# Performance work log

Measured on AMD Instinct MI355X. Metric: run time of the kernel, lower is better.

Reference implementation:

```python
import jax, jax.numpy as jnp
import numpy as np
import math

IN_FEATURES = 256
OUT_FEATURES = 128
B, N = 4, 4096


def setup_inputs() -> dict:
    key = jax.random.key(0)
    ks = jax.random.split(key, 8)
    h = jax.random.normal(ks[0], (B, N, IN_FEATURES), dtype=jnp.float32)
    adj = jax.random.randint(ks[1], (B, N, N), 0, 2, dtype=jnp.int32)
    # Linear params (torch nn.Linear: y = x @ W.T + b)
    s = 1.0 / math.sqrt(IN_FEATURES)
    Wq = jax.random.uniform(ks[2], (OUT_FEATURES, IN_FEATURES), jnp.float32, -s, s)
    bq = jax.random.uniform(ks[3], (OUT_FEATURES,), jnp.float32, -s, s)
    Wk = jax.random.uniform(ks[4], (OUT_FEATURES, IN_FEATURES), jnp.float32, -s, s)
    bk = jax.random.uniform(ks[5], (OUT_FEATURES,), jnp.float32, -s, s)
    Wv = jax.random.uniform(ks[6], (OUT_FEATURES, IN_FEATURES), jnp.float32, -s, s)
    bv = jax.random.uniform(ks[7], (OUT_FEATURES,), jnp.float32, -s, s)
    return {"h": h, "adj": adj, "Wq": Wq, "bq": bq, "Wk": Wk, "bk": bk, "Wv": Wv, "bv": bv}


def reference(h, adj, Wq, bq, Wk, bk, Wv, bv):
    # QKV projections: [B, N, D]
    q = jnp.einsum('bnf,df->bnd', h, Wq) + bq
    k = jnp.einsum('bnf,df->bnd', h, Wk) + bk
    v = jnp.einsum('bnf,df->bnd', h, Wv) + bv
    # Dense scores [B, N, N], scaled
    scores = jnp.einsum('bnd,bmd->bnm', q, k) / math.sqrt(OUT_FEATURES)
    neg = jnp.float32(-9e15)
    scores = jnp.where(adj > 0, scores, neg)
    probs = jax.nn.softmax(scores, axis=-1)
    return jnp.einsum('bnm,bmd->bnd', probs, v)
```

## Files before the change

### kernel.cpp

```cpp
#include <hip/hip_runtime.h>
#include <stdint.h>
#include <math.h>

#define NB 4
#define NN 4096
#define NF 256
#define ND 128
#define KVB 32
#define NR (NB * NN)
#define QKVE ((size_t)NR * ND)

typedef __bf16 bf16x8 __attribute__((ext_vector_type(8)));
typedef __bf16 bf16x4v __attribute__((ext_vector_type(4)));
typedef float f32x4 __attribute__((ext_vector_type(4)));
typedef unsigned short u16x4 __attribute__((ext_vector_type(4)));

__device__ __forceinline__ unsigned short f2bf(float f) {
    union { float f; uint32_t u; } v; v.f = f;
    uint32_t r = (v.u + 0x7FFFu + ((v.u >> 16) & 1u)) >> 16;
    return (unsigned short)r;
}
__device__ __forceinline__ bf16x8 lds_read16(const unsigned short* base, int byte_off) {
    return *reinterpret_cast<const bf16x8*>(reinterpret_cast<const char*>(base) + byte_off);
}
__device__ __forceinline__ void gld_lds16(const void* g, void* l) {
    __builtin_amdgcn_global_load_lds(
        (const __attribute__((address_space(1))) void*)g,
        (__attribute__((address_space(3))) void*)l, 16, 0, 0);
}

__global__ __launch_bounds__(256) void pack_proj(
    const int* __restrict__ adj, unsigned long long* __restrict__ pm64,
    const float* __restrict__ h,
    const float* __restrict__ Wq, const float* __restrict__ bq,
    const float* __restrict__ Wk, const float* __restrict__ bk,
    const float* __restrict__ Wv, const float* __restrict__ bv,
    unsigned short* __restrict__ qo, unsigned short* __restrict__ ko,
    unsigned short* __restrict__ vs, float qscale)
{
    __shared__ unsigned short h_lds[64 * 128];
    __shared__ unsigned short w_lds[128 * 128];

    const int tid = threadIdx.x;
    const int lane = tid & 63;

    if (blockIdx.x < 1024) {
        const int w = tid >> 6;
        const size_t base = ((size_t)blockIdx.x * 4 + w) * 256;
        for (int o = 0; o < 32; ++o) {
            const size_t wb = base + o * 8;
            int v[8];
#pragma unroll
            for (int u = 0; u < 8; ++u)
                v[u] = adj[(wb + u) * 64 + lane];
            unsigned long long m[8];
#pragma unroll
            for (int u = 0; u < 8; ++u)
                m[u] = __ballot(v[u] != 0);
            if (lane == 0) {
#pragma unroll
                for (int u = 0; u < 8; u += 2) {
                    ulonglong2 st; st.x = m[u]; st.y = m[u + 1];
                    *reinterpret_cast<ulonglong2*>(pm64 + wb + u) = st;
                }
            }
        }
        return;
    }

    const int idx = blockIdx.x - 1024;
    const int proj = idx >> 8;
    const int R0 = (idx & 255) * 64;
    const int wv = tid >> 6;
    const int l15 = lane & 15;
    const int lhi = lane >> 4;

    const float* W    = proj == 0 ? Wq : (proj == 1 ? Wk : Wv);
    const float* bias = proj == 0 ? bq : (proj == 1 ? bk : bv);
    const float scale = proj == 0 ? qscale : 1.0f;

    f32x4 acc[8];
#pragma unroll
    for (int i = 0; i < 8; ++i) acc[i] = f32x4{0.f, 0.f, 0.f, 0.f};

    for (int kc = 0; kc < 2; ++kc) {
        const int c0 = kc * 128;
        __syncthreads();
#pragma unroll
        for (int p = 0; p < 8; ++p) {
            int i2 = p * 256 + tid;
            int row = i2 >> 5;
            int seg = i2 & 31;
            f32x4 hv = *reinterpret_cast<const f32x4*>(h + (size_t)(R0 + row) * NF + c0 + seg * 4);
            u16x4 hb;
            hb[0] = f2bf(hv[0]); hb[1] = f2bf(hv[1]); hb[2] = f2bf(hv[2]); hb[3] = f2bf(hv[3]);
            int byte = (row * 256 + seg * 8) ^ ((row & 7) << 4);
            *reinterpret_cast<u16x4*>(reinterpret_cast<char*>(h_lds) + byte) = hb;
        }
#pragma unroll
        for (int p = 0; p < 16; ++p) {
            int i2 = p * 256 + tid;
            int row = i2 >> 5;
            int seg = i2 & 31;
            f32x4 wv4 = *reinterpret_cast<const f32x4*>(W + (size_t)row * NF + c0 + seg * 4);
            u16x4 wb;
            wb[0] = f2bf(wv4[0]); wb[1] = f2bf(wv4[1]); wb[2] = f2bf(wv4[2]); wb[3] = f2bf(wv4[3]);
            int byte = (row * 256 + seg * 8) ^ ((row & 7) << 4);
            *reinterpret_cast<u16x4*>(reinterpret_cast<char*>(w_lds) + byte) = wb;
        }
        __syncthreads();
        const int arow = 16 * wv + l15;
#pragma unroll
        for (int ks = 0; ks < 4; ++ks) {
            int k = ks * 32 + 8 * lhi;
            bf16x8 a = lds_read16(h_lds, (arow * 256 + k * 2) ^ ((arow & 7) << 4));
#pragma unroll
            for (int cs = 0; cs < 8; ++cs) {
                int d = 16 * cs + l15;
                bf16x8 b = lds_read16(w_lds, (d * 256 + k * 2) ^ ((d & 7) << 4));
                acc[cs] = __builtin_amdgcn_mfma_f32_16x16x32_bf16(a, b, acc[cs], 0, 0, 0);
            }
        }
    }
    if (proj < 2) {
        unsigned short* out = proj == 0 ? qo : ko;
#pragma unroll
        for (int cs = 0; cs < 8; ++cs) {
            int d = 16 * cs + l15;
            float bb = bias[d];
#pragma unroll
            for (int j = 0; j < 4; ++j) {
                int row = R0 + 16 * wv + 4 * lhi + j;
                out[(size_t)row * ND + d] = f2bf((acc[cs][j] + bb) * scale);
            }
        }
    } else {
        const int bb_ = R0 >> 12;
        const int nb_ = (R0 & (NN - 1)) + 16 * wv + 4 * lhi;
        const int pt = nb_ >> 5;
        const int ch = (nb_ >> 3) & 3;
        const int mm0 = nb_ & 7;
#pragma unroll
        for (int cs = 0; cs < 8; ++cs) {
            int d = 16 * cs + l15;
            float bb = bias[d];
            u16x4 o;
#pragma unroll
            for (int j = 0; j < 4; ++j) o[j] = f2bf(acc[cs][j] + bb);
            size_t oidx = ((size_t)(bb_ * 128 + pt)) * 4096 + ch * 1024 + d * 8 + mm0;
            *reinterpret_cast<u16x4*>(vs + oidx) = o;
        }
    }
}

__global__ __launch_bounds__(256, 2) void attn(
    const unsigned short* __restrict__ Q,
    const unsigned short* __restrict__ K,
    const unsigned short* __restrict__ VS,
    const unsigned int* __restrict__ pm,
    float* __restrict__ out,
    float* __restrict__ opart1,
    float* __restrict__ ml,
    int ntl)
{
    __shared__ unsigned short stA[8192];
    __shared__ unsigned short stB[8192];
    __shared__ unsigned short p_lds[4096];

    const int tid = threadIdx.x;
    const int lane = tid & 63;
    const int w = tid >> 6;
    const int l15 = lane & 15;
    const int lhi = lane >> 4;

    const int flat = blockIdx.x;
    const int x = flat & 7;
    const int rest = flat >> 3;
    const int qt = rest & 31;
    const int s2 = rest >> 5;
    const int combo = x + 8 * s2;
    const int b = combo & 3;
    const int sp = combo >> 2;
    const int q0w = qt * 128 + w * 32;
    const size_t bN = (size_t)b * NN;
    const int ptbase = sp * ntl;

    const unsigned short* Kb = K + bN * ND;
    const unsigned short* Vbase = VS + (size_t)b * 128 * 4096;

    bf16x8 qf[2][4];
#pragma unroll
    for (int g = 0; g < 2; ++g)
#pragma unroll
        for (int ks = 0; ks < 4; ++ks)
            qf[g][ks] = *reinterpret_cast<const bf16x8*>(
                Q + (bN + q0w + g * 16 + l15) * ND + ks * 32 + 8 * lhi);

    const unsigned int* pmr0 = pm + (bN + (size_t)(q0w + l15)) * 128;
    const unsigned int* pmr1 = pm + (bN + (size_t)(q0w + 16 + l15)) * 128;

    f32x4 acc[2][8];
#pragma unroll
    for (int g = 0; g < 2; ++g)
#pragma unroll
        for (int i = 0; i < 8; ++i) acc[g][i] = f32x4{0.f, 0.f, 0.f, 0.f};
    float m_run[2] = {-INFINITY, -INFINITY};
    float l_part[2] = {0.f, 0.f};

    auto stage = [&](unsigned short* st, int pt) {
        const int m0 = pt * KVB;
#pragma unroll
        for (int i = 0; i < 4; ++i) {
            int c = w * 4 + i;
            if (c < 8) {
                int ms = c >> 2, ks = c & 3;
                const unsigned short* src = Kb
                    + (size_t)(m0 + ms * 16 + l15) * ND + ks * 32 + lhi * 8;
                gld_lds16(src, st + c * 512);
            } else {
                int vi = c - 8;
                const unsigned short* src = Vbase + (size_t)pt * 4096 + vi * 512 + lane * 8;
                gld_lds16(src, st + 4096 + vi * 512);
            }
        }
    };

    auto compute = [&](const unsigned short* st, unsigned int mw0, unsigned int mw1) {
        bf16x8 kf[2][4];
#pragma unroll
        for (int ms = 0; ms < 2; ++ms)
#pragma unroll
            for (int ks = 0; ks < 4; ++ks)
                kf[ms][ks] = lds_read16(st, (ms * 4 + ks) * 1024 + lane * 16);

        f32x4 s[2][2];
#pragma unroll
        for (int g = 0; g < 2; ++g)
#pragma unroll
            for (int ms = 0; ms < 2; ++ms) s[g][ms] = f32x4{0.f, 0.f, 0.f, 0.f};
        __builtin_amdgcn_s_setprio(1);
#pragma unroll
        for (int g = 0; g < 2; ++g)
#pragma unroll
            for (int ms = 0; ms < 2; ++ms)
#pragma unroll
                for (int ks = 0; ks < 4; ++ks)
                    s[g][ms] = __builtin_amdgcn_mfma_f32_16x16x32_bf16(
                        kf[ms][ks], qf[g][ks], s[g][ms], 0, 0, 0);
        __builtin_amdgcn_s_setprio(0);

        bf16x8 vf[8];
#pragma unroll
        for (int ds = 0; ds < 8; ++ds)
            vf[ds] = lds_read16(st + 4096, lhi * 2048 + ds * 256 + l15 * 16);

        const unsigned int mw[2] = {mw0, mw1};
        float smaxl[2];
        float dmax = -INFINITY;
#pragma unroll
        for (int g = 0; g < 2; ++g) {
            unsigned int mwg = mw[g] >> (4 * lhi);
#pragma unroll
            for (int ms = 0; ms < 2; ++ms)
#pragma unroll
                for (int r = 0; r < 4; ++r)
                    if (!((mwg >> (16 * ms + r)) & 1u)) s[g][ms][r] = -1.0e30f;
            float mx = fmaxf(fmaxf(fmaxf(s[g][0][0], s[g][0][1]), fmaxf(s[g][0][2], s[g][0][3])),
                             fmaxf(fmaxf(s[g][1][0], s[g][1][1]), fmaxf(s[g][1][2], s[g][1][3])));
            smaxl[g] = mx;
            dmax = fmaxf(dmax, mx - m_run[g]);
        }
        if (!__all(dmax <= 8.0f)) {
#pragma unroll
            for (int g = 0; g < 2; ++g) {
                float mx = smaxl[g];
                mx = fmaxf(mx, __shfl_xor(mx, 16, 64));
                mx = fmaxf(mx, __shfl_xor(mx, 32, 64));
                float mnew = fmaxf(m_run[g], mx);
                float c = exp2f(m_run[g] - mnew);
                m_run[g] = mnew;
                l_part[g] *= c;
#pragma unroll
                for (int ds = 0; ds < 8; ++ds) acc[g][ds] *= c;
            }
        }

#pragma unroll
        for (int g = 0; g < 2; ++g) {
            bf16x4v pbv[2];
#pragma unroll
            for (int ms = 0; ms < 2; ++ms)
#pragma unroll
                for (int r = 0; r < 4; ++r) {
                    float p = exp2f(s[g][ms][r] - m_run[g]);
                    __bf16 pb = (__bf16)p;
                    l_part[g] += (float)pb;
                    pbv[ms][r] = pb;
                }
            const int base = (w * 2 + g) * 1024 + l15 * 64;
#pragma unroll
            for (int ms = 0; ms < 2; ++ms)
                *reinterpret_cast<bf16x4v*>(reinterpret_cast<char*>(p_lds)
                    + base + ms * 32 + lhi * 8) = pbv[ms];
            bf16x8 pa = lds_read16(p_lds, base + lhi * 16);
            __builtin_amdgcn_s_setprio(1);
#pragma unroll
            for (int ds = 0; ds < 8; ++ds)
                acc[g][ds] = __builtin_amdgcn_mfma_f32_16x16x32_bf16(
                    vf[ds], pa, acc[g][ds], 0, 0, 0);
            __builtin_amdgcn_s_setprio(0);
        }
    };

    stage(stA, ptbase);
    __syncthreads();

    uint4 mk[2], mk2[2];
    mk[0] = *reinterpret_cast<const uint4*>(pmr0 + ptbase);
    mk[1] = *reinterpret_cast<const uint4*>(pmr1 + ptbase);
    for (int t = 0; t < ntl; t += 4) {
        int tn4 = (t + 4 < ntl) ? t + 4 : t;
        mk2[0] = *reinterpret_cast<const uint4*>(pmr0 + ptbase + tn4);
        mk2[1] = *reinterpret_cast<const uint4*>(pmr1 + ptbase + tn4);

        stage(stB, ptbase + t + 1);
        compute(stA, mk[0].x, mk[1].x);
        __syncthreads();
        stage(stA, ptbase + t + 2 < ptbase + ntl ? ptbase + t + 2 : ptbase + ntl - 1);
        compute(stB, mk[0].y, mk[1].y);
        __syncthreads();
        stage(stB, ptbase + t + 3 < ptbase + ntl ? ptbase + t + 3 : ptbase + ntl - 1);
        compute(stA, mk[0].z, mk[1].z);
        __syncthreads();
        stage(stA, ptbase + (t + 4 < ntl ? t + 4 : ntl - 1));
        compute(stB, mk[0].w, mk[1].w);
        __syncthreads();

        mk[0] = mk2[0]; mk[1] = mk2[1];
    }

#pragma unroll
    for (int g = 0; g < 2; ++g) {
        float rs = l_part[g];
        rs += __shfl_xor(rs, 16, 64);
        rs += __shfl_xor(rs, 32, 64);
        l_part[g] = rs;
    }

    float* op = (sp == 0) ? out : (opart1 + (size_t)(sp - 1) * NR * ND);
#pragma unroll
    for (int g = 0; g < 2; ++g) {
        const size_t rowbase = (bN + q0w + g * 16 + l15) * ND;
#pragma unroll
        for (int ds = 0; ds < 8; ++ds)
            *reinterpret_cast<f32x4*>(op + rowbase + 16 * ds + 4 * lhi) = acc[g][ds];
    }
    if (lhi == 0) {
#pragma unroll
        for (int g = 0; g < 2; ++g) {
            size_t gr = bN + q0w + g * 16 + l15;
            *reinterpret_cast<float2*>(ml + ((size_t)sp * NR + gr) * 2) =
                make_float2(m_run[g], l_part[g]);
        }
    }
}

__global__ __launch_bounds__(256) void merge_splits(
    float* __restrict__ out, const float* __restrict__ opart1,
    const float* __restrict__ ml, int nsplit)
{
    int idx = blockIdx.x * 256 + threadIdx.x;
    int row = idx >> 5;
    int d4 = (idx & 31) * 4;
    float mmax = ml[(size_t)row * 2];
    for (int sp = 1; sp < nsplit; ++sp)
        mmax = fmaxf(mmax, ml[((size_t)sp * NR + row) * 2]);
    f32x4 o0 = *reinterpret_cast<const f32x4*>(out + (size_t)row * ND + d4);
    float w0 = exp2f(ml[(size_t)row * 2] - mmax);
    float lsum = ml[(size_t)row * 2 + 1] * w0;
    f32x4 acc;
#pragma unroll
    for (int j = 0; j < 4; ++j) acc[j] = o0[j] * w0;
    for (int sp = 1; sp < nsplit; ++sp) {
        float m_s = ml[((size_t)sp * NR + row) * 2];
        float l_s = ml[((size_t)sp * NR + row) * 2 + 1];
        float ws_ = exp2f(m_s - mmax);
        f32x4 os = *reinterpret_cast<const f32x4*>(opart1 + ((size_t)(sp - 1) * NR + row) * ND + d4);
#pragma unroll
        for (int j = 0; j < 4; ++j) acc[j] += os[j] * ws_;
        lsum += l_s * ws_;
    }
    float inv = 1.0f / lsum;
    f32x4 r;
#pragma unroll
    for (int j = 0; j < 4; ++j) r[j] = acc[j] * inv;
    *reinterpret_cast<f32x4*>(out + (size_t)row * ND + d4) = r;
}

extern "C" void kernel_launch(void* const* d_in, const int* in_sizes, int n_in,
                              void* d_out, int out_size, void* d_ws, size_t ws_size,
                              hipStream_t stream) {
    const float* h  = (const float*)d_in[0];
    const int* adj  = (const int*)d_in[1];
    const float* Wq = (const float*)d_in[2];
    const float* bq = (const float*)d_in[3];
    const float* Wk = (const float*)d_in[4];
    const float* bk = (const float*)d_in[5];
    const float* Wv = (const float*)d_in[6];
    const float* bv = (const float*)d_in[7];
    float* out = (float*)d_out;

    unsigned short* qws  = (unsigned short*)d_ws;
    unsigned short* kws  = qws + QKVE;
    unsigned short* vsws = kws + QKVE;
    float* opart1 = (float*)(vsws + QKVE);

    const size_t pm_bytes = (size_t)NB * NN * (NN / 8);
    const size_t need4 = 3 * QKVE * 2 + 3 * QKVE * 4 + 4 * (size_t)NR * 2 * 4 + pm_bytes;
    const int nsplit = (ws_size >= need4) ? 4 : 2;
    float* mlws = opart1 + (size_t)(nsplit - 1) * NR * ND;
    unsigned int* pmws = (unsigned int*)(mlws + (size_t)nsplit * NR * 2);
    const int ntl = (NN / KVB) / nsplit;

    const float qscale = (float)(0.08838834764831845 / 0.6931471805599453);

    pack_proj<<<dim3(1024 + 768), 256, 0, stream>>>(
        adj, (unsigned long long*)pmws,
        h, Wq, bq, Wk, bk, Wv, bv, qws, kws, vsws, qscale);
    attn<<<dim3(32 * 4 * nsplit), 256, 0, stream>>>(
        qws, kws, vsws, pmws, out, opart1, mlws, ntl);
    merge_splits<<<dim3(NR * 32 / 256), 256, 0, stream>>>(out, opart1, mlws, nsplit);
}
```

Measured before the change: 152.8 us.

## Split KV range six ways with uneven tile counts and raise occupancy

Raises the attention KV split from 4 to 6 when workspace allows, giving 768 blocks instead of 512. The 128 KV tiles are divided unevenly (22,22,22,22,20,20), and the main loop is unrolled by 2 instead of 4 so those counts divide evenly. Launch bounds now target 3 blocks per SM, which may limit registers and cause spills. The aim is better CU fill on MI355X; the cost is extra partial outputs to write and merge.

```diff
diff --git a/kernel.cpp b/kernel.cpp
--- a/kernel.cpp
+++ b/kernel.cpp
@@ -153,7 +153,7 @@
     }
 }
 
-__global__ __launch_bounds__(256, 2) void attn(
+__global__ __launch_bounds__(256, 3) void attn(
     const unsigned short* __restrict__ Q,
     const unsigned short* __restrict__ K,
     const unsigned short* __restrict__ VS,
@@ -161,7 +161,7 @@
     float* __restrict__ out,
     float* __restrict__ opart1,
     float* __restrict__ ml,
-    int ntl)
+    int nsplit)
 {
     __shared__ unsigned short stA[8192];
     __shared__ unsigned short stB[8192];
@@ -177,13 +177,20 @@
     const int x = flat & 7;
     const int rest = flat >> 3;
     const int qt = rest & 31;
-    const int s2 = rest >> 5;
-    const int combo = x + 8 * s2;
+    const int s3 = rest >> 5;
+    const int combo = x + 8 * s3;
     const int b = combo & 3;
     const int sp = combo >> 2;
     const int q0w = qt * 128 + w * 32;
     const size_t bN = (size_t)b * NN;
-    const int ptbase = sp * ntl;
+
+    int ptbase, ntl;
+    if (nsplit == 6) {
+        if (sp < 4) { ptbase = 22 * sp; ntl = 22; }
+        else        { ptbase = 88 + 20 * (sp - 4); ntl = 20; }
+    } else {
+        ntl = 128 / nsplit; ptbase = sp * ntl;
+    }
 
     const unsigned short* Kb = K + bN * ND;
     const unsigned short* Vbase = VS + (size_t)b * 128 * 4096;
@@ -315,28 +322,21 @@
     stage(stA, ptbase);
     __syncthreads();
 
-    uint4 mk[2], mk2[2];
-    mk[0] = *reinterpret_cast<const uint4*>(pmr0 + ptbase);
-    mk[1] = *reinterpret_cast<const uint4*>(pmr1 + ptbase);
-    for (int t = 0; t < ntl; t += 4) {
-        int tn4 = (t + 4 < ntl) ? t + 4 : t;
-        mk2[0] = *reinterpret_cast<const uint4*>(pmr0 + ptbase + tn4);
-        mk2[1] = *reinterpret_cast<const uint4*>(pmr1 + ptbase + tn4);
+    uint2 mk0 = *reinterpret_cast<const uint2*>(pmr0 + ptbase);
+    uint2 mk1 = *reinterpret_cast<const uint2*>(pmr1 + ptbase);
+    for (int t = 0; t < ntl; t += 2) {
+        int tn = (t + 2 < ntl) ? t + 2 : t;
+        uint2 nk0 = *reinterpret_cast<const uint2*>(pmr0 + ptbase + tn);
+        uint2 nk1 = *reinterpret_cast<const uint2*>(pmr1 + ptbase + tn);
 
         stage(stB, ptbase + t + 1);
-        compute(stA, mk[0].x, mk[1].x);
+        compute(stA, mk0.x, mk1.x);
         __syncthreads();
-        stage(stA, ptbase + t + 2 < ptbase + ntl ? ptbase + t + 2 : ptbase + ntl - 1);
-        compute(stB, mk[0].y, mk[1].y);
+        stage(stA, ptbase + (t + 2 < ntl ? t + 2 : ntl - 1));
+        compute(stB, mk0.y, mk1.y);
         __syncthreads();
-        stage(stB, ptbase + t + 3 < ptbase + ntl ? ptbase + t + 3 : ptbase + ntl - 1);
-        compute(stA, mk[0].z, mk[1].z);
-        __syncthreads();
-        stage(stA, ptbase + (t + 4 < ntl ? t + 4 : ntl - 1));
-        compute(stB, mk[0].w, mk[1].w);
-        __syncthreads();
-
-        mk[0] = mk2[0]; mk[1] = mk2[1];
+
+        mk0 = nk0; mk1 = nk1;
     }
 
 #pragma unroll
@@ -416,11 +416,11 @@
     float* opart1 = (float*)(vsws + QKVE);
 
     const size_t pm_bytes = (size_t)NB * NN * (NN / 8);
+    const size_t need6 = 3 * QKVE * 2 + 5 * QKVE * 4 + 6 * (size_t)NR * 2 * 4 + pm_bytes;
     const size_t need4 = 3 * QKVE * 2 + 3 * QKVE * 4 + 4 * (size_t)NR * 2 * 4 + pm_bytes;
-    const int nsplit = (ws_size >= need4) ? 4 : 2;
+    const int nsplit = (ws_size >= need6) ? 6 : ((ws_size >= need4) ? 4 : 2);
     float* mlws = opart1 + (size_t)(nsplit - 1) * NR * ND;
     unsigned int* pmws = (unsigned int*)(mlws + (size_t)nsplit * NR * 2);
-    const int ntl = (NN / KVB) / nsplit;
 
     const float qscale = (float)(0.08838834764831845 / 0.6931471805599453);
 
@@ -428,6 +428,6 @@
         adj, (unsigned long long*)pmws,
         h, Wq, bq, Wk, bk, Wv, bv, qws, kws, vsws, qscale);
     attn<<<dim3(32 * 4 * nsplit), 256, 0, stream>>>(
-        qws, kws, vsws, pmws, out, opart1, mlws, ntl);
+        qws, kws, vsws, pmws, out, opart1, mlws, nsplit);
     merge_splits<<<dim3(NR * 32 / 256), 256, 0, stream>>>(out, opart1, mlws, nsplit);
 }
```

After: 217.0 us. +42.0%, slower.

## Restructure KV double-buffer loop with explicit partial waitcnt and raw barriers

Applied to the files above, without the earlier changes.

Replaces the four-way unrolled stage/compute loop with a two-stage body that issues the next tile's stage and per-tile mask loads, then waits only with vmcnt(6) before an s_barrier, so the newest global loads can stay in flight during compute. Mask words are now loaded one tile at a time instead of as uint4 groups of four. Sched barriers pin instruction order around the raw barriers. The hand-picked vmcnt value must match the number of loads issued, and it does not drain LDS writes the way __syncthreads would, which risks races if the counts or lgkm ordering are wrong.

```diff
diff --git a/kernel.cpp b/kernel.cpp
--- a/kernel.cpp
+++ b/kernel.cpp
@@ -312,31 +312,29 @@
         }
     };
 
+    auto body = [&](unsigned short* cur, unsigned short* nxt,
+                    unsigned int (&mkc)[2], unsigned int (&mkn)[2], int t) {
+        int tn = (t + 1 < ntl) ? t + 1 : ntl - 1;
+        stage(nxt, ptbase + tn);
+        mkn[0] = pmr0[ptbase + tn];
+        mkn[1] = pmr1[ptbase + tn];
+        asm volatile("s_waitcnt vmcnt(6)" ::: "memory");
+        __builtin_amdgcn_sched_barrier(0);
+        __builtin_amdgcn_s_barrier();
+        __builtin_amdgcn_sched_barrier(0);
+        compute(cur, mkc[0], mkc[1]);
+        __builtin_amdgcn_sched_barrier(0);
+        __builtin_amdgcn_s_barrier();
+        __builtin_amdgcn_sched_barrier(0);
+    };
+
+    unsigned int muA[2], muB[2];
     stage(stA, ptbase);
-    __syncthreads();
-
-    uint4 mk[2], mk2[2];
-    mk[0] = *reinterpret_cast<const uint4*>(pmr0 + ptbase);
-    mk[1] = *reinterpret_cast<const uint4*>(pmr1 + ptbase);
-    for (int t = 0; t < ntl; t += 4) {
-        int tn4 = (t + 4 < ntl) ? t + 4 : t;
-        mk2[0] = *reinterpret_cast<const uint4*>(pmr0 + ptbase + tn4);
-        mk2[1] = *reinterpret_cast<const uint4*>(pmr1 + ptbase + tn4);
-
-        stage(stB, ptbase + t + 1);
-        compute(stA, mk[0].x, mk[1].x);
-        __syncthreads();
-        stage(stA, ptbase + t + 2 < ptbase + ntl ? ptbase + t + 2 : ptbase + ntl - 1);
-        compute(stB, mk[0].y, mk[1].y);
-        __syncthreads();
-        stage(stB, ptbase + t + 3 < ptbase + ntl ? ptbase + t + 3 : ptbase + ntl - 1);
-        compute(stA, mk[0].z, mk[1].z);
-        __syncthreads();
-        stage(stA, ptbase + (t + 4 < ntl ? t + 4 : ntl - 1));
-        compute(stB, mk[0].w, mk[1].w);
-        __syncthreads();
-
-        mk[0] = mk2[0]; mk[1] = mk2[1];
+    muA[0] = pmr0[ptbase];
+    muA[1] = pmr1[ptbase];
+    for (int t = 0; t < ntl; t += 2) {
+        body(stA, stB, muA, muB, t);
+        body(stB, stA, muB, muA, t + 1);
     }
 
 #pragma unroll
```

After: 159.7 us. 4.6% more time.

## Halve query rows per warp in attention to raise occupancy and block count

Applied to the files above, without the earlier changes.

Each warp in the attention kernel now handles 16 query rows instead of 32, so a block covers 64 rows and the grid doubles. Register state (accumulators, Q fragments, K/V fragments) shrinks and launch bounds ask for 4 blocks per CU, trading K/V reuse across rows for more concurrent waves. K and V fragments are now loaded from LDS just before each MFMA instead of being preloaded, and the tile loop is unrolled by 2 instead of 4. Each K/V tile is staged into LDS twice as often overall, so global and LDS traffic per output row goes up.

```diff
diff --git a/kernel.cpp b/kernel.cpp
--- a/kernel.cpp
+++ b/kernel.cpp
@@ -153,7 +153,7 @@
     }
 }
 
-__global__ __launch_bounds__(256, 2) void attn(
+__global__ __launch_bounds__(256, 4) void attn(
     const unsigned short* __restrict__ Q,
     const unsigned short* __restrict__ K,
     const unsigned short* __restrict__ VS,
@@ -165,7 +165,7 @@
 {
     __shared__ unsigned short stA[8192];
     __shared__ unsigned short stB[8192];
-    __shared__ unsigned short p_lds[4096];
+    __shared__ unsigned short p_lds[2048];
 
     const int tid = threadIdx.x;
     const int lane = tid & 63;
@@ -176,36 +176,31 @@
     const int flat = blockIdx.x;
     const int x = flat & 7;
     const int rest = flat >> 3;
-    const int qt = rest & 31;
-    const int s2 = rest >> 5;
+    const int qt = rest & 63;
+    const int s2 = rest >> 6;
     const int combo = x + 8 * s2;
     const int b = combo & 3;
     const int sp = combo >> 2;
-    const int q0w = qt * 128 + w * 32;
+    const int q0w = qt * 64 + w * 16;
     const size_t bN = (size_t)b * NN;
     const int ptbase = sp * ntl;
 
     const unsigned short* Kb = K + bN * ND;
     const unsigned short* Vbase = VS + (size_t)b * 128 * 4096;
 
-    bf16x8 qf[2][4];
-#pragma unroll
-    for (int g = 0; g < 2; ++g)
-#pragma unroll
-        for (int ks = 0; ks < 4; ++ks)
-            qf[g][ks] = *reinterpret_cast<const bf16x8*>(
-                Q + (bN + q0w + g * 16 + l15) * ND + ks * 32 + 8 * lhi);
-
-    const unsigned int* pmr0 = pm + (bN + (size_t)(q0w + l15)) * 128;
-    const unsigned int* pmr1 = pm + (bN + (size_t)(q0w + 16 + l15)) * 128;
-
-    f32x4 acc[2][8];
-#pragma unroll
-    for (int g = 0; g < 2; ++g)
-#pragma unroll
-        for (int i = 0; i < 8; ++i) acc[g][i] = f32x4{0.f, 0.f, 0.f, 0.f};
-    float m_run[2] = {-INFINITY, -INFINITY};
-    float l_part[2] = {0.f, 0.f};
+    bf16x8 qf[4];
+#pragma unroll
+    for (int ks = 0; ks < 4; ++ks)
+        qf[ks] = *reinterpret_cast<const bf16x8*>(
+            Q + (bN + q0w + l15) * ND + ks * 32 + 8 * lhi);
+
+    const unsigned int* pmr = pm + (bN + (size_t)(q0w + l15)) * 128;
+
+    f32x4 acc[8];
+#pragma unroll
+    for (int i = 0; i < 8; ++i) acc[i] = f32x4{0.f, 0.f, 0.f, 0.f};
+    float m_run = -INFINITY;
+    float l_part = 0.f;
 
     auto stage = [&](unsigned short* st, int pt) {
         const int m0 = pt * KVB;
@@ -225,143 +220,99 @@
         }
     };
 
-    auto compute = [&](const unsigned short* st, unsigned int mw0, unsigned int mw1) {
-        bf16x8 kf[2][4];
-#pragma unroll
-        for (int ms = 0; ms < 2; ++ms)
-#pragma unroll
-            for (int ks = 0; ks < 4; ++ks)
-                kf[ms][ks] = lds_read16(st, (ms * 4 + ks) * 1024 + lane * 16);
-
-        f32x4 s[2][2];
-#pragma unroll
-        for (int g = 0; g < 2; ++g)
-#pragma unroll
-            for (int ms = 0; ms < 2; ++ms) s[g][ms] = f32x4{0.f, 0.f, 0.f, 0.f};
+    auto compute = [&](const unsigned short* st, unsigned int mw) {
+        f32x4 s0 = f32x4{0.f, 0.f, 0.f, 0.f}, s1 = f32x4{0.f, 0.f, 0.f, 0.f};
         __builtin_amdgcn_s_setprio(1);
-#pragma unroll
-        for (int g = 0; g < 2; ++g)
-#pragma unroll
-            for (int ms = 0; ms < 2; ++ms)
-#pragma unroll
-                for (int ks = 0; ks < 4; ++ks)
-                    s[g][ms] = __builtin_amdgcn_mfma_f32_16x16x32_bf16(
-                        kf[ms][ks], qf[g][ks], s[g][ms], 0, 0, 0);
+        {
+#pragma unroll
+            for (int ks = 0; ks < 4; ++ks) {
+                bf16x8 kf = lds_read16(st, ks * 1024 + lane * 16);
+                s0 = __builtin_amdgcn_mfma_f32_16x16x32_bf16(kf, qf[ks], s0, 0, 0, 0);
+            }
+#pragma unroll
+            for (int ks = 0; ks < 4; ++ks) {
+                bf16x8 kf = lds_read16(st, (4 + ks) * 1024 + lane * 16);
+                s1 = __builtin_amdgcn_mfma_f32_16x16x32_bf16(kf, qf[ks], s1, 0, 0, 0);
+            }
+        }
         __builtin_amdgcn_s_setprio(0);
 
-        bf16x8 vf[8];
-#pragma unroll
-        for (int ds = 0; ds < 8; ++ds)
-            vf[ds] = lds_read16(st + 4096, lhi * 2048 + ds * 256 + l15 * 16);
-
-        const unsigned int mw[2] = {mw0, mw1};
-        float smaxl[2];
-        float dmax = -INFINITY;
-#pragma unroll
-        for (int g = 0; g < 2; ++g) {
-            unsigned int mwg = mw[g] >> (4 * lhi);
-#pragma unroll
-            for (int ms = 0; ms < 2; ++ms)
-#pragma unroll
-                for (int r = 0; r < 4; ++r)
-                    if (!((mwg >> (16 * ms + r)) & 1u)) s[g][ms][r] = -1.0e30f;
-            float mx = fmaxf(fmaxf(fmaxf(s[g][0][0], s[g][0][1]), fmaxf(s[g][0][2], s[g][0][3])),
-                             fmaxf(fmaxf(s[g][1][0], s[g][1][1]), fmaxf(s[g][1][2], s[g][1][3])));
-            smaxl[g] = mx;
-            dmax = fmaxf(dmax, mx - m_run[g]);
-        }
-        if (!__all(dmax <= 8.0f)) {
-#pragma unroll
-            for (int g = 0; g < 2; ++g) {
-                float mx = smaxl[g];
-                mx = fmaxf(mx, __shfl_xor(mx, 16, 64));
-                mx = fmaxf(mx, __shfl_xor(mx, 32, 64));
-                float mnew = fmaxf(m_run[g], mx);
-                float c = exp2f(m_run[g] - mnew);
-                m_run[g] = mnew;
-                l_part[g] *= c;
-#pragma unroll
-                for (int ds = 0; ds < 8; ++ds) acc[g][ds] *= c;
-            }
-        }
-
-#pragma unroll
-        for (int g = 0; g < 2; ++g) {
-            bf16x4v pbv[2];
-#pragma unroll
-            for (int ms = 0; ms < 2; ++ms)
-#pragma unroll
-                for (int r = 0; r < 4; ++r) {
-                    float p = exp2f(s[g][ms][r] - m_run[g]);
-                    __bf16 pb = (__bf16)p;
-                    l_part[g] += (float)pb;
-                    pbv[ms][r] = pb;
-                }
-            const int base = (w * 2 + g) * 1024 + l15 * 64;
-#pragma unroll
-            for (int ms = 0; ms < 2; ++ms)
-                *reinterpret_cast<bf16x4v*>(reinterpret_cast<char*>(p_lds)
-                    + base + ms * 32 + lhi * 8) = pbv[ms];
-            bf16x8 pa = lds_read16(p_lds, base + lhi * 16);
-            __builtin_amdgcn_s_setprio(1);
-#pragma unroll
-            for (int ds = 0; ds < 8; ++ds)
-                acc[g][ds] = __builtin_amdgcn_mfma_f32_16x16x32_bf16(
-                    vf[ds], pa, acc[g][ds], 0, 0, 0);
-            __builtin_amdgcn_s_setprio(0);
-        }
+        unsigned int mwg = mw >> (4 * lhi);
+#pragma unroll
+        for (int r = 0; r < 4; ++r) {
+            if (!((mwg >> r) & 1u))        s0[r] = -1.0e30f;
+            if (!((mwg >> (16 + r)) & 1u)) s1[r] = -1.0e30f;
+        }
+        float mx = fmaxf(fmaxf(fmaxf(s0[0], s0[1]), fmaxf(s0[2], s0[3])),
+                         fmaxf(fmaxf(s1[0], s1[1]), fmaxf(s1[2], s1[3])));
+        if (!__all(mx - m_run <= 8.0f)) {
+            mx = fmaxf(mx, __shfl_xor(mx, 16, 64));
+            mx = fmaxf(mx, __shfl_xor(mx, 32, 64));
+            float mnew = fmaxf(m_run, mx);
+            float c = exp2f(m_run - mnew);
+            m_run = mnew;
+            l_part *= c;
+#pragma unroll
+            for (int ds = 0; ds < 8; ++ds) acc[ds] *= c;
+        }
+
+        bf16x4v pbv0, pbv1;
+#pragma unroll
+        for (int r = 0; r < 4; ++r) {
+            float p0 = exp2f(s0[r] - m_run);
+            float p1 = exp2f(s1[r] - m_run);
+            __bf16 b0 = (__bf16)p0, b1 = (__bf16)p1;
+            l_part += (float)b0 + (float)b1;
+            pbv0[r] = b0; pbv1[r] = b1;
+        }
+        const int base = w * 1024 + l15 * 64;
+        *reinterpret_cast<bf16x4v*>(reinterpret_cast<char*>(p_lds) + base + lhi * 8) = pbv0;
+        *reinterpret_cast<bf16x4v*>(reinterpret_cast<char*>(p_lds) + base + 32 + lhi * 8) = pbv1;
+        bf16x8 pa = lds_read16(p_lds, base + lhi * 16);
+
+        __builtin_amdgcn_s_setprio(1);
+#pragma unroll
+        for (int ds = 0; ds < 8; ++ds) {
+            bf16x8 vf = lds_read16(st + 4096, lhi * 2048 + ds * 256 + l15 * 16);
+            acc[ds] = __builtin_amdgcn_mfma_f32_16x16x32_bf16(vf, pa, acc[ds], 0, 0, 0);
+        }
+        __builtin_amdgcn_s_setprio(0);
     };
 
     stage(stA, ptbase);
     __syncthreads();
 
-    uint4 mk[2], mk2[2];
-    mk[0] = *reinterpret_cast<const uint4*>(pmr0 + ptbase);
-    mk[1] = *reinterpret_cast<const uint4*>(pmr1 + ptbase);
-    for (int t = 0; t < ntl; t += 4) {
-        int tn4 = (t + 4 < ntl) ? t + 4 : t;
-        mk2[0] = *reinterpret_cast<const uint4*>(pmr0 + ptbase + tn4);
-        mk2[1] = *reinterpret_cast<const uint4*>(pmr1 + ptbase + tn4);
+    uint2 mk = *reinterpret_cast<const uint2*>(pmr + ptbase);
+    for (int t = 0; t < ntl; t += 2) {
+        int tn = (t + 2 < ntl) ? t + 2 : t;
+        uint2 nk = *reinterpret_cast<const uint2*>(pmr + ptbase + tn);
 
         stage(stB, ptbase + t + 1);
-        compute(stA, mk[0].x, mk[1].x);
+        compute(stA, mk.x);
         __syncthreads();
-        stage(stA, ptbase + t + 2 < ptbase + ntl ? ptbase + t + 2 : ptbase + ntl - 1);
-        compute(stB, mk[0].y, mk[1].y);
+        stage(stA, ptbase + (t + 2 < ntl ? t + 2 : ntl - 1));
+        compute(stB, mk.y);
         __syncthreads();
-        stage(stB, ptbase + t + 3 < ptbase + ntl ? ptbase + t + 3 : ptbase + ntl - 1);
-        compute(stA, mk[0].z, mk[1].z);
-        __syncthreads();
-        stage(stA, ptbase + (t + 4 < ntl ? t + 4 : ntl - 1));
-        compute(stB, mk[0].w, mk[1].w);
-        __syncthreads();
-
-        mk[0] = mk2[0]; mk[1] = mk2[1];
-    }
-
-#pragma unroll
-    for (int g = 0; g < 2; ++g) {
-        float rs = l_part[g];
+
+        mk = nk;
+    }
+
+    {
+        float rs = l_part;
         rs += __shfl_xor(rs, 16, 64);
         rs += __shfl_xor(rs, 32, 64);
-        l_part[g] = rs;
+        l_part = rs;
     }
 
     float* op = (sp == 0) ? out : (opart1 + (size_t)(sp - 1) * NR * ND);
-#pragma unroll
-    for (int g = 0; g < 2; ++g) {
-        const size_t rowbase = (bN + q0w + g * 16 + l15) * ND;
-#pragma unroll
-        for (int ds = 0; ds < 8; ++ds)
-            *reinterpret_cast<f32x4*>(op + rowbase + 16 * ds + 4 * lhi) = acc[g][ds];
-    }
+    const size_t rowbase = (bN + q0w + l15) * ND;
+#pragma unroll
+    for (int ds = 0; ds < 8; ++ds)
+        *reinterpret_cast<f32x4*>(op + rowbase + 16 * ds + 4 * lhi) = acc[ds];
     if (lhi == 0) {
-#pragma unroll
-        for (int g = 0; g < 2; ++g) {
-            size_t gr = bN + q0w + g * 16 + l15;
-            *reinterpret_cast<float2*>(ml + ((size_t)sp * NR + gr) * 2) =
-                make_float2(m_run[g], l_part[g]);
-        }
+        size_t gr = bN + q0w + l15;
+        *reinterpret_cast<float2*>(ml + ((size_t)sp * NR + gr) * 2) =
+            make_float2(m_run, l_part);
     }
 }
 
@@ -427,7 +378,7 @@
     pack_proj<<<dim3(1024 + 768), 256, 0, stream>>>(
         adj, (unsigned long long*)pmws,
         h, Wq, bq, Wk, bk, Wv, bv, qws, kws, vsws, qscale);
-    attn<<<dim3(32 * 4 * nsplit), 256, 0, stream>>>(
+    attn<<<dim3(64 * 4 * nsplit), 256, 0, stream>>>(
         qws, kws, vsws, pmws, out, opart1, mlws, ntl);
     merge_splits<<<dim3(NR * 32 / 256), 256, 0, stream>>>(out, opart1, mlws, nsplit);
 }
```

Result: slower. 155.8 us (+2.0%).
